# Optimization experiments

Measured on AMD Instinct MI355X. Metric: run time of the kernel, lower is better.

The kernel has to match this reference:

```python
import jax, jax.numpy as jnp
import numpy as np


def setup_inputs() -> dict:
    key = jax.random.key(0)
    k1, k2, k3, k4, k5 = jax.random.split(key, 5)
    B, F, E, NF = 16384, 1024, 64, 32
    return {
        "input": jax.random.normal(k1, (B, F), dtype=jnp.float32),
        "fields": jax.random.randint(k2, (F,), 0, NF, dtype=jnp.int32),
        "w_weight": jax.random.normal(k3, (1, F), dtype=jnp.float32) * 0.02,
        "w_bias": jax.random.normal(k4, (1,), dtype=jnp.float32) * 0.02,
        "vs": jax.random.normal(k5, (NF, F, E), dtype=jnp.float32) * 0.05,
    }


def reference(input, fields, w_weight, w_bias, vs):
    # Linear (1st-order) term: [B, 1]
    linear = input @ w_weight.T + w_bias

    F = input.shape[1]
    # Gather field-aware embedding tables per feature: G[k, i, e] = vs[fields[k], i, e]
    G = vs[fields]  # [F, F, E]
    # A[i, j] = dot(vs[fields[j], i, :], vs[fields[i], j, :])
    A = jnp.einsum("jie,ije->ij", G, G)  # [F, F]
    # P[i, j] = sum_b input[b, i] * input[b, j]  (original sums over batch)
    P = input.T @ input  # [F, F]
    # second_order = sum_{i < j} A[i, j] * P[i, j]  (scalar, as in the source)
    second_order = jnp.sum(jnp.triu(A * P, k=1))

    return jax.nn.sigmoid(linear + second_order)
```

## Files before the change

kernel.cpp:

```cpp
#include <hip/hip_runtime.h>
#include <hip/hip_fp16.h>
#include <math.h>
#include <stdint.h>

#define FDIM 1024
#define BTOT 16384
#define EDIM 64
#define NFLD 32
#define NPANEL 4
#define NPAIRS 10

typedef _Float16 half8 __attribute__((ext_vector_type(8)));
typedef __fp16 fp16x2 __attribute__((ext_vector_type(2)));
typedef float f32x4 __attribute__((ext_vector_type(4)));

__device__ __forceinline__ uint32_t pk2(float a, float b){
  fp16x2 h = __builtin_amdgcn_cvt_pkrtz(a, b);
  return __builtin_bit_cast(uint32_t, h);
}

__device__ __forceinline__ float fget(const float4& v, int i){
  switch (i){ case 0: return v.x; case 1: return v.y; case 2: return v.z; default: return v.w; }
}

__device__ __forceinline__ int pairId(int ti, int tj){
  return ti * NPANEL - (ti * (ti + 1)) / 2 + tj;
}

__device__ __forceinline__ int CMAP(int col){
  return ((col & 3) << 6) | ((col >> 2) ^ ((col & 3) << 1));
}

__global__ __launch_bounds__(256) void w2_kernel(
    const float* __restrict__ vs, const int* __restrict__ fields,
    _Float16* __restrict__ Wp){
  __shared__ float Si[32][68];
  __shared__ float Sj[32][68];
  __shared__ int gI[32], gJ[32];
  __shared__ int cnt[NFLD], pos[NFLD], off[NFLD + 1];
  __shared__ int permS[FDIM];
  const int t = threadIdx.x;

  if (t < NFLD) cnt[t] = 0;
  __syncthreads();
#pragma unroll
  for (int r = 0; r < 4; ++r) atomicAdd(&cnt[fields[t + 256 * r]], 1);
  __syncthreads();
  if (t == 0){
    int s = 0;
    for (int i = 0; i < NFLD; ++i){ off[i] = s; s += cnt[i]; }
    off[NFLD] = s;
  }
  __syncthreads();
  if (t < NFLD) pos[t] = off[t];
  __syncthreads();
#pragma unroll
  for (int r = 0; r < 4; ++r){
    const int idx = t + 256 * r;
    const int p = atomicAdd(&pos[fields[idx]], 1);
    permS[p] = idx;
  }
  __syncthreads();

  const int a = blockIdx.x >> 5, b = blockIdx.x & 31;
  const int oa = off[a], na = off[a + 1] - oa;
  const int ob = off[b], nb_ = off[b + 1] - ob;
  if (na == 0 || nb_ == 0) return;
  for (int ia0 = 0; ia0 < na; ia0 += 32){
    const int nac = min(32, na - ia0);
    for (int jb0 = 0; jb0 < nb_; jb0 += 32){
      const int nbc = min(32, nb_ - jb0);
      __syncthreads();
      if (t < 32){
        gI[t] = (t < nac) ? permS[oa + ia0 + t] : 0;
        gJ[t] = (t < nbc) ? permS[ob + jb0 + t] : 0;
      }
      __syncthreads();
#pragma unroll
      for (int rep = 0; rep < 2; ++rep){
        const int lidx = rep * 256 + t;
        const int r = lidx >> 4, e4 = (lidx & 15) * 4;
        if (r < nac)
          *(float4*)&Si[r][e4] = *(const float4*)(vs + ((size_t)b * FDIM + gI[r]) * EDIM + e4);
        if (r < nbc)
          *(float4*)&Sj[r][e4] = *(const float4*)(vs + ((size_t)a * FDIM + gJ[r]) * EDIM + e4);
      }
      __syncthreads();
      const int jr = t & 31;
      const int ir0 = t >> 5;
      for (int ko = 0; ko * 8 < nac; ++ko){
        const int ir = ko * 8 + ir0;
        if (ir < nac && jr < nbc){
          float dot = 0.f;
#pragma unroll
          for (int e4 = 0; e4 < EDIM; e4 += 4){
            const float4 x = *(const float4*)&Si[ir][e4];
            const float4 y = *(const float4*)&Sj[jr][e4];
            dot += x.x * y.x + x.y * y.y + x.z * y.z + x.w * y.w;
          }
          const int gi = gI[ir], gj = gJ[jr];
          const int pi = gi >> 8, pj = gj >> 8;
          if (pi <= pj){
            const float v = (gj > gi) ? dot : 0.f;
            const int li = gi & 255, lj = gj & 255;
            const int P  = pairId(pi, pj);
            const int w8 = (li >> 7) * 4 + (lj >> 6);
            const int mb = (li >> 4) & 7, r_ = li & 3;
            const int lane = ((li >> 2) & 3) * 16 + (lj & 15);
            const int nbv = (lj >> 4) & 3;
            const size_t o_ = (size_t)(P * 8 + w8) * 8192
                            + (size_t)((mb * 2 + (r_ >> 1)) * 64 + lane) * 8
                            + (r_ & 1) * 4 + nbv;
            Wp[o_] = (_Float16)v;
          }
        }
      }
    }
  }
}

__global__ __launch_bounds__(512, 1) void gram_fx(
    const float* __restrict__ X, const float* __restrict__ w,
    const _Float16* __restrict__ Wp,
    float* __restrict__ partial, float* __restrict__ lin){
  __shared__ uint4 lds4[8192];
  const int t = threadIdx.x, wv = t >> 6, lane = t & 63;
  const int orow = lane >> 4, rl = lane & 15;
  const int wr = wv >> 2, wc = wv & 3;
  const int k0 = blockIdx.x * 64 + wv * 8;

  float lp[8];
#pragma unroll
  for (int r = 0; r < 8; ++r) lp[r] = 0.f;

#pragma unroll 1
  for (int p = 0; p < NPANEL; ++p){
    const int c0 = p * 256;
    float4 rv[8];
#pragma unroll
    for (int r = 0; r < 8; ++r)
      rv[r] = *(const float4*)(X + (size_t)(k0 + r) * FDIM + c0 + 4 * lane);
    const float4 w4 = *(const float4*)(w + c0 + 4 * lane);
#pragma unroll
    for (int r = 0; r < 8; ++r)
      lp[r] += rv[r].x * w4.x + rv[r].y * w4.y + rv[r].z * w4.z + rv[r].w * w4.w;

    uint4* base = lds4 + wv * 1024 + p * 256;
#pragma unroll
    for (int i = 0; i < 4; ++i){
      uint4 ch;
      ch.x = pk2(fget(rv[0], i), fget(rv[1], i));
      ch.y = pk2(fget(rv[2], i), fget(rv[3], i));
      ch.z = pk2(fget(rv[4], i), fget(rv[5], i));
      ch.w = pk2(fget(rv[6], i), fget(rv[7], i));
      base[(i << 6) | (lane ^ (i << 1))] = ch;
    }
  }

#pragma unroll
  for (int r = 0; r < 8; ++r){
    float v = lp[r];
#pragma unroll
    for (int off = 32; off; off >>= 1) v += __shfl_xor(v, off, 64);
    if (lane == 0) lin[k0 + r] = v;
  }

  __syncthreads();

  int swA[8], swB[4];
#pragma unroll
  for (int mb = 0; mb < 8; ++mb) swA[mb] = CMAP(wr * 128 + mb * 16 + rl);
#pragma unroll
  for (int nb = 0; nb < 4; ++nb) swB[nb] = CMAP(wc * 64 + nb * 16 + rl);

  float wsum = 0.f;

  auto loadB = [&](int tj, half8 (&bf)[2][4]){
#pragma unroll
    for (int s = 0; s < 2; ++s)
#pragma unroll
      for (int nb = 0; nb < 4; ++nb)
        bf[s][nb] = __builtin_bit_cast(half8,
            lds4[(s * 4 + orow) * 1024 + tj * 256 + swB[nb]]);
  };

  auto body = [&](int ti, int tj, const half8 (&bf)[2][4]){
    if (ti == tj && wr == 1 && wc < 2) return;

    const uint4* wp = (const uint4*)(Wp + (size_t)(pairId(ti, tj) * 8 + wv) * 8192);
    half8 wreg[16];
#pragma unroll
    for (int q = 0; q < 16; ++q)
      wreg[q] = __builtin_bit_cast(half8, wp[q * 64 + lane]);

    f32x4 acc[8][4];
#pragma unroll
    for (int i = 0; i < 8; ++i)
#pragma unroll
      for (int j = 0; j < 4; ++j) acc[i][j] = {0.f, 0.f, 0.f, 0.f};
#pragma unroll
    for (int s = 0; s < 2; ++s)
#pragma unroll
      for (int mb = 0; mb < 8; ++mb){
        const half8 af = __builtin_bit_cast(half8,
            lds4[(s * 4 + orow) * 1024 + ti * 256 + swA[mb]]);
#pragma unroll
        for (int nb = 0; nb < 4; ++nb)
          acc[mb][nb] = __builtin_amdgcn_mfma_f32_16x16x32_f16(
              af, bf[s][nb], acc[mb][nb], 0, 0, 0);
      }
#pragma unroll
    for (int mb = 0; mb < 8; ++mb)
#pragma unroll
      for (int h = 0; h < 2; ++h){
        const half8 hv = wreg[mb * 2 + h];
#pragma unroll
        for (int r2 = 0; r2 < 2; ++r2)
#pragma unroll
          for (int nb = 0; nb < 4; ++nb)
            wsum += (float)hv[r2 * 4 + nb] * acc[mb][nb][2 * h + r2];
      }
  };

#pragma unroll 1
  for (int G = 0; G < NPANEL; ++G){
    half8 bf[2][4];
    loadB(G, bf);
#pragma unroll 1
    for (int ti = 0; ti <= G; ++ti) body(ti, G, bf);
  }

#pragma unroll
  for (int off = 32; off; off >>= 1) wsum += __shfl_xor(wsum, off, 64);
  __syncthreads();
  float* red = (float*)lds4;
  if (lane == 0) red[wv] = wsum;
  __syncthreads();
  if (t == 0){
    float s = 0.f;
#pragma unroll
    for (int i = 0; i < 8; ++i) s += red[i];
    partial[blockIdx.x] = s;
  }
}

__global__ __launch_bounds__(256) void final_out(
    const float* __restrict__ partial, const float* __restrict__ lin,
    const float* __restrict__ wb, float* __restrict__ out){
  __shared__ float red[256];
  const int t = threadIdx.x;
  red[t] = partial[t];
  __syncthreads();
  for (int off = 128; off; off >>= 1){
    if (t < off) red[t] += red[t + off];
    __syncthreads();
  }
  const float stot = red[0] + wb[0];
  const int i = blockIdx.x * 256 + t;
  const float z = lin[i] + stot;
  out[i] = 1.f / (1.f + expf(-z));
}

extern "C" void kernel_launch(void* const* d_in, const int* in_sizes, int n_in,
                              void* d_out, int out_size, void* d_ws,
                              size_t ws_size, hipStream_t stream) {
  const float* X      = (const float*)d_in[0];
  const int* fields   = (const int*)d_in[1];
  const float* ww     = (const float*)d_in[2];
  const float* wbias  = (const float*)d_in[3];
  const float* vs     = (const float*)d_in[4];
  float* out          = (float*)d_out;

  char* ws = (char*)d_ws;
  float* partial = (float*)ws;
  float* lin = (float*)(ws + (64 << 10));
  _Float16* Wp = (_Float16*)(ws + (size_t)(4 << 20));


  w2_kernel<<<NFLD * NFLD, 256, 0, stream>>>(vs, fields, Wp);
  gram_fx<<<256, 512, 0, stream>>>(X, ww, Wp, partial, lin);
  final_out<<<BTOT / 256, 256, 0, stream>>>(partial, lin, wbias, out);
}
```

Measured before the change: 61.17 us.

## Double gram kernel block to 16 waves with smaller per-wave tiles

Grows the gram kernel from 8 to 16 waves per block. Each wave now computes a 64x64 tile instead of 128x64 of each 256x256 panel pair, and the W weight layout produced by w2_kernel is re-tiled to match. Loading X is split across wave pairs, with the linear-term partials written into two buffers that final_out sums. Diagonal panels now skip all strictly-lower wave tiles, and the scalar accumulator is split into four to shorten the dependency chain. The aim is more latency hiding and less per-wave register pressure, at the cost of more B-fragment LDS reloads per block.

```diff
diff --git a/kernel.cpp b/kernel.cpp
--- a/kernel.cpp
+++ b/kernel.cpp
@@ -104,11 +104,11 @@
             const float v = (gj > gi) ? dot : 0.f;
             const int li = gi & 255, lj = gj & 255;
             const int P  = pairId(pi, pj);
-            const int w8 = (li >> 7) * 4 + (lj >> 6);
-            const int mb = (li >> 4) & 7, r_ = li & 3;
+            const int w16 = ((li >> 6) << 2) | (lj >> 6);
+            const int mb = (li >> 4) & 3, r_ = li & 3;
             const int lane = ((li >> 2) & 3) * 16 + (lj & 15);
             const int nbv = (lj >> 4) & 3;
-            const size_t o_ = (size_t)(P * 8 + w8) * 8192
+            const size_t o_ = (size_t)(P * 16 + w16) * 4096
                             + (size_t)((mb * 2 + (r_ >> 1)) * 64 + lane) * 8
                             + (r_ & 1) * 4 + nbv;
             Wp[o_] = (_Float16)v;
@@ -119,61 +119,66 @@
   }
 }
 
-__global__ __launch_bounds__(512, 1) void gram_fx(
+__global__ __launch_bounds__(1024, 1) void gram_fx(
     const float* __restrict__ X, const float* __restrict__ w,
     const _Float16* __restrict__ Wp,
-    float* __restrict__ partial, float* __restrict__ lin){
+    float* __restrict__ partial, float* __restrict__ linp){
   __shared__ uint4 lds4[8192];
   const int t = threadIdx.x, wv = t >> 6, lane = t & 63;
   const int orow = lane >> 4, rl = lane & 15;
   const int wr = wv >> 2, wc = wv & 3;
-  const int k0 = blockIdx.x * 64 + wv * 8;
-
-  float lp[8];
-#pragma unroll
-  for (int r = 0; r < 8; ++r) lp[r] = 0.f;
+
+  {
+    const int o  = wv >> 1;
+    const int ph = wv & 1;
+    const int k0 = blockIdx.x * 64 + o * 8;
+    float lp[8];
+#pragma unroll
+    for (int r = 0; r < 8; ++r) lp[r] = 0.f;
 
 #pragma unroll 1
-  for (int p = 0; p < NPANEL; ++p){
-    const int c0 = p * 256;
-    float4 rv[8];
-#pragma unroll
-    for (int r = 0; r < 8; ++r)
-      rv[r] = *(const float4*)(X + (size_t)(k0 + r) * FDIM + c0 + 4 * lane);
-    const float4 w4 = *(const float4*)(w + c0 + 4 * lane);
-#pragma unroll
-    for (int r = 0; r < 8; ++r)
-      lp[r] += rv[r].x * w4.x + rv[r].y * w4.y + rv[r].z * w4.z + rv[r].w * w4.w;
-
-    uint4* base = lds4 + wv * 1024 + p * 256;
-#pragma unroll
-    for (int i = 0; i < 4; ++i){
-      uint4 ch;
-      ch.x = pk2(fget(rv[0], i), fget(rv[1], i));
-      ch.y = pk2(fget(rv[2], i), fget(rv[3], i));
-      ch.z = pk2(fget(rv[4], i), fget(rv[5], i));
-      ch.w = pk2(fget(rv[6], i), fget(rv[7], i));
-      base[(i << 6) | (lane ^ (i << 1))] = ch;
+    for (int pp = 0; pp < 2; ++pp){
+      const int p = ph * 2 + pp;
+      const int c0 = p * 256;
+      float4 rv[8];
+#pragma unroll
+      for (int r = 0; r < 8; ++r)
+        rv[r] = *(const float4*)(X + (size_t)(k0 + r) * FDIM + c0 + 4 * lane);
+      const float4 w4 = *(const float4*)(w + c0 + 4 * lane);
+#pragma unroll
+      for (int r = 0; r < 8; ++r)
+        lp[r] += rv[r].x * w4.x + rv[r].y * w4.y + rv[r].z * w4.z + rv[r].w * w4.w;
+
+      uint4* base = lds4 + o * 1024 + p * 256;
+#pragma unroll
+      for (int i = 0; i < 4; ++i){
+        uint4 ch;
+        ch.x = pk2(fget(rv[0], i), fget(rv[1], i));
+        ch.y = pk2(fget(rv[2], i), fget(rv[3], i));
+        ch.z = pk2(fget(rv[4], i), fget(rv[5], i));
+        ch.w = pk2(fget(rv[6], i), fget(rv[7], i));
+        base[(i << 6) | (lane ^ (i << 1))] = ch;
+      }
     }
-  }
-
-#pragma unroll
-  for (int r = 0; r < 8; ++r){
-    float v = lp[r];
-#pragma unroll
-    for (int off = 32; off; off >>= 1) v += __shfl_xor(v, off, 64);
-    if (lane == 0) lin[k0 + r] = v;
-  }
-
-  __syncthreads();
-
-  int swA[8], swB[4];
-#pragma unroll
-  for (int mb = 0; mb < 8; ++mb) swA[mb] = CMAP(wr * 128 + mb * 16 + rl);
+
+#pragma unroll
+    for (int r = 0; r < 8; ++r){
+      float v = lp[r];
+#pragma unroll
+      for (int off = 32; off; off >>= 1) v += __shfl_xor(v, off, 64);
+      if (lane == 0) linp[(size_t)ph * BTOT + k0 + r] = v;
+    }
+  }
+
+  __syncthreads();
+
+  int swA[4], swB[4];
+#pragma unroll
+  for (int mb = 0; mb < 4; ++mb) swA[mb] = CMAP(wr * 64 + mb * 16 + rl);
 #pragma unroll
   for (int nb = 0; nb < 4; ++nb) swB[nb] = CMAP(wc * 64 + nb * 16 + rl);
 
-  float wsum = 0.f;
+  float ws4[4] = {0.f, 0.f, 0.f, 0.f};
 
   auto loadB = [&](int tj, half8 (&bf)[2][4]){
 #pragma unroll
@@ -185,23 +190,23 @@
   };
 
   auto body = [&](int ti, int tj, const half8 (&bf)[2][4]){
-    if (ti == tj && wr == 1 && wc < 2) return;
-
-    const uint4* wp = (const uint4*)(Wp + (size_t)(pairId(ti, tj) * 8 + wv) * 8192);
-    half8 wreg[16];
-#pragma unroll
-    for (int q = 0; q < 16; ++q)
+    if (ti == tj && wr > wc) return;
+
+    const uint4* wp = (const uint4*)(Wp + (size_t)(pairId(ti, tj) * 16 + wv) * 4096);
+    half8 wreg[8];
+#pragma unroll
+    for (int q = 0; q < 8; ++q)
       wreg[q] = __builtin_bit_cast(half8, wp[q * 64 + lane]);
 
-    f32x4 acc[8][4];
-#pragma unroll
-    for (int i = 0; i < 8; ++i)
+    f32x4 acc[4][4];
+#pragma unroll
+    for (int i = 0; i < 4; ++i)
 #pragma unroll
       for (int j = 0; j < 4; ++j) acc[i][j] = {0.f, 0.f, 0.f, 0.f};
 #pragma unroll
     for (int s = 0; s < 2; ++s)
 #pragma unroll
-      for (int mb = 0; mb < 8; ++mb){
+      for (int mb = 0; mb < 4; ++mb){
         const half8 af = __builtin_bit_cast(half8,
             lds4[(s * 4 + orow) * 1024 + ti * 256 + swA[mb]]);
 #pragma unroll
@@ -210,7 +215,7 @@
               af, bf[s][nb], acc[mb][nb], 0, 0, 0);
       }
 #pragma unroll
-    for (int mb = 0; mb < 8; ++mb)
+    for (int mb = 0; mb < 4; ++mb)
 #pragma unroll
       for (int h = 0; h < 2; ++h){
         const half8 hv = wreg[mb * 2 + h];
@@ -218,7 +223,7 @@
         for (int r2 = 0; r2 < 2; ++r2)
 #pragma unroll
           for (int nb = 0; nb < 4; ++nb)
-            wsum += (float)hv[r2 * 4 + nb] * acc[mb][nb][2 * h + r2];
+            ws4[nb] += (float)hv[r2 * 4 + nb] * acc[mb][nb][2 * h + r2];
       }
   };
 
@@ -230,6 +235,8 @@
     for (int ti = 0; ti <= G; ++ti) body(ti, G, bf);
   }
 
+  float wsum = (ws4[0] + ws4[1]) + (ws4[2] + ws4[3]);
+
 #pragma unroll
   for (int off = 32; off; off >>= 1) wsum += __shfl_xor(wsum, off, 64);
   __syncthreads();
@@ -239,13 +246,13 @@
   if (t == 0){
     float s = 0.f;
 #pragma unroll
-    for (int i = 0; i < 8; ++i) s += red[i];
+    for (int i = 0; i < 16; ++i) s += red[i];
     partial[blockIdx.x] = s;
   }
 }
 
 __global__ __launch_bounds__(256) void final_out(
-    const float* __restrict__ partial, const float* __restrict__ lin,
+    const float* __restrict__ partial, const float* __restrict__ linp,
     const float* __restrict__ wb, float* __restrict__ out){
   __shared__ float red[256];
   const int t = threadIdx.x;
@@ -257,7 +264,7 @@
   }
   const float stot = red[0] + wb[0];
   const int i = blockIdx.x * 256 + t;
-  const float z = lin[i] + stot;
+  const float z = linp[i] + linp[BTOT + i] + stot;
   out[i] = 1.f / (1.f + expf(-z));
 }
 
@@ -273,11 +280,11 @@
 
   char* ws = (char*)d_ws;
   float* partial = (float*)ws;
-  float* lin = (float*)(ws + (64 << 10));
+  float* linp = (float*)(ws + (64 << 10));
   _Float16* Wp = (_Float16*)(ws + (size_t)(4 << 20));
 
 
   w2_kernel<<<NFLD * NFLD, 256, 0, stream>>>(vs, fields, Wp);
-  gram_fx<<<256, 512, 0, stream>>>(X, ww, Wp, partial, lin);
-  final_out<<<BTOT / 256, 256, 0, stream>>>(partial, lin, wbias, out);
-}
+  gram_fx<<<256, 1024, 0, stream>>>(X, ww, Wp, partial, linp);
+  final_out<<<BTOT / 256, 256, 0, stream>>>(partial, linp, wbias, out);
+}
```

Result: slower. 74.38 us (+21.6%).
